# Kernel optimization log

Measured on AMD Instinct MI355X. Metric: run time of the kernel, lower is better.

The kernel has to match this reference:

```python
import jax, jax.numpy as jnp
import numpy as np

B, S, D, H, W = 2, 2048, 1024, 16, 256
HD = D // H

def setup_inputs() -> dict:
    key = jax.random.key(0)
    k1, k2, k3 = jax.random.split(key, 3)
    x = jax.random.normal(k1, (B, S, D), dtype=jnp.float32)
    w_qkv = jax.random.normal(k2, (D, 3 * D), dtype=jnp.float32) * (D ** -0.5)
    b_qkv = jnp.zeros((3 * D,), dtype=jnp.float32)
    w_out = jax.random.normal(k3, (D, D), dtype=jnp.float32) * (D ** -0.5)
    b_out = jnp.zeros((D,), dtype=jnp.float32)
    return {"x": x, "w_qkv": w_qkv, "b_qkv": b_qkv, "w_out": w_out, "b_out": b_out}

def reference(x, w_qkv, b_qkv, w_out, b_out):
    b, s, d = x.shape
    qkv = x @ w_qkv + b_qkv                       # [B,S,3D]
    qkv = qkv.reshape(b, s, 3, H, HD)
    q = jnp.transpose(qkv[:, :, 0], (0, 2, 1, 3))  # [B,H,S,HD]
    k = jnp.transpose(qkv[:, :, 1], (0, 2, 1, 3))
    v = jnp.transpose(qkv[:, :, 2], (0, 2, 1, 3))
    # NOTE: original scales by d_model**0.5, not head_dim**0.5
    scores = jnp.einsum('bhqd,bhkd->bhqk', q, k) / (d ** 0.5)
    idx = jnp.arange(s)
    band = jnp.abs(idx[:, None] - idx[None, :]) <= W  # |i-j| <= window_size
    scores = jnp.where(band[None, None], scores, -jnp.inf)
    attn = jax.nn.softmax(scores, axis=-1)
    out = jnp.einsum('bhqk,bhkd->bhqd', attn, v)
    out = jnp.transpose(out, (0, 2, 1, 3)).reshape(b, s, d)
    return out @ w_out + b_out
```

## Files before the change

kernel.cpp:

```cpp
#include <hip/hip_runtime.h>
#include <cstdint>
#include <cmath>

typedef unsigned short u16;
typedef __attribute__((ext_vector_type(8))) short bf16x8;
typedef __attribute__((ext_vector_type(4))) float f32x4;
typedef __attribute__((ext_vector_type(8))) unsigned short u16x8;
typedef __attribute__((ext_vector_type(4))) unsigned short u16x4;

#define DEV static __device__ __forceinline__

DEV u16 f2bf(float f) {
  union { float f; uint32_t u; } v; v.f = f;
  uint32_t r = (v.u + 0x7fffu + ((v.u >> 16) & 1u)) >> 16;
  return (u16)r;
}

DEV float fexp2(float x) { return exp2f(x); }

DEV void async16(void* lds, const void* g) {
  __builtin_amdgcn_global_load_lds(
      (const __attribute__((address_space(1))) uint32_t*)g,
      (__attribute__((address_space(3))) uint32_t*)lds, 16, 0, 0);
}

#define QSCALE 0.04508422002778011f

__global__ void conv8(const float* __restrict__ in, u16* __restrict__ out, int n8) {
  int i = blockIdx.x * 256 + threadIdx.x;
  if (i >= n8) return;
  const float4* p = (const float4*)in + (size_t)i * 2;
  float4 a = p[0], b = p[1];
  u16x8 ov;
  ov[0] = f2bf(a.x); ov[1] = f2bf(a.y); ov[2] = f2bf(a.z); ov[3] = f2bf(a.w);
  ov[4] = f2bf(b.x); ov[5] = f2bf(b.y); ov[6] = f2bf(b.z); ov[7] = f2bf(b.w);
  *(u16x8*)(out + (size_t)i * 8) = ov;
}

__global__ void tconv(const float* __restrict__ in, u16* __restrict__ out, int R, int Cdim) {
  __shared__ float t[32][33];
  const int tx = threadIdx.x & 31, ty = threadIdx.x >> 5;
  const int r0 = blockIdx.y * 32, c0 = blockIdx.x * 32;
#pragma unroll
  for (int k = 0; k < 4; ++k) {
    int r = ty + k * 8;
    t[r][tx] = in[(size_t)(r0 + r) * Cdim + c0 + tx];
  }
  __syncthreads();
#pragma unroll
  for (int k = 0; k < 4; ++k) {
    int cc = ty + k * 8;
    out[(size_t)(c0 + cc) * R + r0 + tx] = f2bf(t[tx][cc]);
  }
}

template <int EPI>
__global__ __launch_bounds__(256, 2) void gemm_bt(
    const u16* __restrict__ A, const u16* __restrict__ BT,
    const float* __restrict__ bias, float* __restrict__ C,
    u16* __restrict__ qb, u16* __restrict__ kbuf, u16* __restrict__ vtb,
    int Mdim, int Ndim, int Kdim)
{
  __shared__ u16 Alds[128 * 64];
  __shared__ u16 Blds[128 * 64];
  const int tid = threadIdx.x;
  const int wid = tid >> 6, lane = tid & 63;
  const int g = lane >> 4, c = lane & 15;
  const int wr = wid >> 1, wc = wid & 1;
  const int gx = gridDim.x;
  const int nwg = gx * gridDim.y;
  const int lin = blockIdx.y * gx + blockIdx.x;
  const int work = (lin & 7) * (nwg >> 3) + (lin >> 3);
  const int row0 = (work / gx) * 128, col0 = (work % gx) * 128;

  f32x4 acc[4][4] = {};

  for (int kt = 0; kt < Kdim; kt += 64) {
    __syncthreads();
#pragma unroll
    for (int it = 0; it < 4; ++it) {
      int chunk = wid * 256 + it * 64 + lane;
      int r = chunk >> 3, j = chunk & 7;
      int js = j ^ (r & 7);
      async16((char*)Alds + (wid * 256 + it * 64) * 16,
              A + (size_t)(row0 + r) * Kdim + kt + js * 8);
      async16((char*)Blds + (wid * 256 + it * 64) * 16,
              BT + (size_t)(col0 + r) * Kdim + kt + js * 8);
    }
    __syncthreads();
#pragma unroll
    for (int kk = 0; kk < 2; ++kk) {
      bf16x8 av[4], bv[4];
#pragma unroll
      for (int mi = 0; mi < 4; ++mi) {
        int r = wr * 64 + mi * 16 + c;
        int js = (kk * 4 + g) ^ (r & 7);
        av[mi] = *(const bf16x8*)((const char*)Alds + r * 128 + js * 16);
      }
#pragma unroll
      for (int ni = 0; ni < 4; ++ni) {
        int r = wc * 64 + ni * 16 + c;
        int js = (kk * 4 + g) ^ (r & 7);
        bv[ni] = *(const bf16x8*)((const char*)Blds + r * 128 + js * 16);
      }
#pragma unroll
      for (int mi = 0; mi < 4; ++mi)
#pragma unroll
        for (int ni = 0; ni < 4; ++ni)
          acc[mi][ni] = __builtin_amdgcn_mfma_f32_16x16x32_bf16(
              av[mi], bv[ni], acc[mi][ni], 0, 0, 0);
    }
  }

#pragma unroll
  for (int mi = 0; mi < 4; ++mi) {
#pragma unroll
    for (int ni = 0; ni < 4; ++ni) {
      int colg = col0 + wc * 64 + ni * 16 + c;
      float bsv = bias[colg];
      int rowb = row0 + wr * 64 + mi * 16 + g * 4;
      if (EPI == 0) {
#pragma unroll
        for (int r = 0; r < 4; ++r)
          C[(size_t)(rowb + r) * Ndim + colg] = acc[mi][ni][r] + bsv;
      } else {
        int t = colg >> 10, rem = colg & 1023;
        int h = rem >> 6, hd = rem & 63;
        int b = rowb >> 11, s0 = rowb & 2047;
        size_t bho = (size_t)(b * 16 + h);
        if (t == 2) {
          u16x4 pv;
#pragma unroll
          for (int r = 0; r < 4; ++r) pv[r] = f2bf(acc[mi][ni][r] + bsv);
          *(u16x4*)(vtb + (bho * 64 + hd) * 2048 + s0) = pv;
        } else {
          u16* dst = (t == 0) ? qb : kbuf;
          float sc = (t == 0) ? QSCALE : 1.0f;
#pragma unroll
          for (int r = 0; r < 4; ++r)
            dst[(bho * 2048 + (s0 + r)) * 64 + hd] = f2bf((acc[mi][ni][r] + bsv) * sc);
        }
      }
    }
  }
}

__global__ __launch_bounds__(512, 4) void attn_win(
    const u16* __restrict__ qb, const u16* __restrict__ kb,
    const u16* __restrict__ vtb, u16* __restrict__ hb)
{
  constexpr int S = 2048, W = 256;
  __shared__ u16 Klds[3][64 * 64];
  __shared__ u16 Vlds[3][64 * 64];
  __shared__ u16 Plds[8][16 * 64];

  const int tid = threadIdx.x, wid = tid >> 6, lane = tid & 63;
  const int g = lane >> 4, c = lane & 15;
  const int lin = blockIdx.x;
  const int work = (lin & 7) * 64 + (lin >> 3);
  const int qt = work & 15, bh = work >> 4;
  const int q0 = qt * 128;
  const int qr0 = q0 + wid * 16;
  const int qw = qr0 + c;
  const size_t bho = (size_t)bh * S * 64;

  bf16x8 aq[2];
  {
    const u16* qrow = qb + bho + (size_t)qw * 64;
    aq[0] = *(const bf16x8*)(qrow + g * 8);
    aq[1] = *(const bf16x8*)(qrow + 32 + g * 8);
  }
  f32x4 o[4] = {};
  float m = -1e30f, lsum = 0.f;

  const int kstart = (q0 - W > 0) ? (q0 - W) : 0;
  const int kend = (q0 + 128 + W < S) ? (q0 + 128 + W) : S;
  const int ntiles = (kend - kstart) >> 6;

  const int sr = tid >> 3, sj = tid & 7;
  const int sjs = sj ^ (sr & 7);
#define STAGE(buf, k0s)                                                         \
  {                                                                             \
    async16((char*)&Klds[buf][0] + tid * 16,                                    \
            kb + bho + (size_t)((k0s) + sr) * 64 + sjs * 8);                    \
    async16((char*)&Vlds[buf][0] + tid * 16,                                    \
            vtb + bho + (size_t)sr * S + (k0s) + sjs * 8);                      \
  }

  STAGE(0, kstart);
  if (ntiles > 1) STAGE(1, kstart + 64);

  for (int i = 0; i < ntiles; ++i) {
    const int k0 = kstart + (i << 6);
    if (i + 1 < ntiles) { asm volatile("s_waitcnt vmcnt(2)" ::: "memory"); }
    else                { asm volatile("s_waitcnt vmcnt(0)" ::: "memory"); }
    __builtin_amdgcn_s_barrier();
    __builtin_amdgcn_sched_barrier(0);
    if (i + 2 < ntiles) STAGE((i + 2) % 3, k0 + 128);

    const int cur = i % 3;
    const bool wave_active = !(k0 > qr0 + 15 + W) && !(k0 + 63 < qr0 - W);
    if (wave_active) {
      const u16* Kb = &Klds[cur][0];
      const u16* Vb = &Vlds[cur][0];

      f32x4 sacc[4] = {};
      __builtin_amdgcn_s_setprio(1);
#pragma unroll
      for (int kb4 = 0; kb4 < 4; ++kb4) {
        int krow = kb4 * 16 + c;
#pragma unroll
        for (int kk = 0; kk < 2; ++kk) {
          int js = (kk * 4 + g) ^ (krow & 7);
          bf16x8 bk = *(const bf16x8*)((const char*)Kb + krow * 128 + js * 16);
          sacc[kb4] = __builtin_amdgcn_mfma_f32_16x16x32_bf16(bk, aq[kk], sacc[kb4], 0, 0, 0);
        }
      }
      __builtin_amdgcn_s_setprio(0);

      const bool full = (k0 >= qr0 + 15 - W) && (k0 + 63 <= qr0 + W);
      float sl[4][4];
      if (full) {
#pragma unroll
        for (int kb4 = 0; kb4 < 4; ++kb4)
#pragma unroll
          for (int r = 0; r < 4; ++r) sl[kb4][r] = sacc[kb4][r];
      } else {
#pragma unroll
        for (int kb4 = 0; kb4 < 4; ++kb4) {
#pragma unroll
          for (int r = 0; r < 4; ++r) {
            int key = k0 + kb4 * 16 + g * 4 + r;
            int d = qw - key;
            bool valid = (d <= W) && (d >= -W);
            sl[kb4][r] = valid ? sacc[kb4][r] : -1e30f;
          }
        }
      }

      float mx = fmaxf(
          fmaxf(fmaxf(fmaxf(sl[0][0], sl[0][1]), fmaxf(sl[0][2], sl[0][3])),
                fmaxf(fmaxf(sl[1][0], sl[1][1]), fmaxf(sl[1][2], sl[1][3]))),
          fmaxf(fmaxf(fmaxf(sl[2][0], sl[2][1]), fmaxf(sl[2][2], sl[2][3])),
                fmaxf(fmaxf(sl[3][0], sl[3][1]), fmaxf(sl[3][2], sl[3][3]))));
      mx = fmaxf(mx, __shfl_xor(mx, 16));
      mx = fmaxf(mx, __shfl_xor(mx, 32));

      if (!__all(mx - m <= 8.0f)) {
        float mnew = fmaxf(m, mx);
        float fs = fexp2(m - mnew);
        m = mnew;
        lsum *= fs;
        float fsr[4];
#pragma unroll
        for (int r = 0; r < 4; ++r)
          fsr[r] = __shfl(fs, (lane & 48) | (((lane & 48) >> 2) + r));
#pragma unroll
        for (int nb = 0; nb < 4; ++nb)
#pragma unroll
          for (int r = 0; r < 4; ++r) o[nb][r] *= fsr[r];
      }

      float rsum = 0.f;
      u16* Pw = &Plds[wid][0];
#pragma unroll
      for (int kb4 = 0; kb4 < 4; ++kb4) {
        float p0, p1, p2, p3;
        if (full) {
          p0 = fexp2(sl[kb4][0] - m); p1 = fexp2(sl[kb4][1] - m);
          p2 = fexp2(sl[kb4][2] - m); p3 = fexp2(sl[kb4][3] - m);
        } else {
          p0 = (sl[kb4][0] > -1e29f) ? fexp2(sl[kb4][0] - m) : 0.f;
          p1 = (sl[kb4][1] > -1e29f) ? fexp2(sl[kb4][1] - m) : 0.f;
          p2 = (sl[kb4][2] > -1e29f) ? fexp2(sl[kb4][2] - m) : 0.f;
          p3 = (sl[kb4][3] > -1e29f) ? fexp2(sl[kb4][3] - m) : 0.f;
        }
        rsum += (p0 + p1) + (p2 + p3);
        uint32_t lo, hi;
        asm("v_cvt_pk_bf16_f32 %0, %1, %2" : "=v"(lo) : "v"(p0), "v"(p1));
        asm("v_cvt_pk_bf16_f32 %0, %1, %2" : "=v"(hi) : "v"(p2), "v"(p3));
        uint2 wv; wv.x = lo; wv.y = hi;
        *(uint2*)((char*)Pw + c * 128 + (((kb4 * 2 + (g >> 1)) ^ (c & 7)) << 4) +
                  ((g & 1) << 3)) = wv;
      }
      rsum += __shfl_xor(rsum, 16);
      rsum += __shfl_xor(rsum, 32);
      lsum += rsum;

      asm volatile("s_waitcnt lgkmcnt(0)" ::: "memory");
      __builtin_amdgcn_sched_barrier(0);
      __builtin_amdgcn_s_setprio(1);
#pragma unroll
      for (int ks = 0; ks < 2; ++ks) {
        int js = (ks * 4 + g) ^ (c & 7);
        bf16x8 pa = *(const bf16x8*)((const char*)Pw + c * 128 + js * 16);
#pragma unroll
        for (int nb = 0; nb < 4; ++nb) {
          int hd = nb * 16 + c;
          int vjs = (ks * 4 + g) ^ (hd & 7);
          bf16x8 bv = *(const bf16x8*)((const char*)Vb + hd * 128 + vjs * 16);
          o[nb] = __builtin_amdgcn_mfma_f32_16x16x32_bf16(pa, bv, o[nb], 0, 0, 0);
        }
      }
      __builtin_amdgcn_s_setprio(0);
    }
  }
#undef STAGE

  const int b = bh >> 4, h = bh & 15;
  float linv[4];
#pragma unroll
  for (int r = 0; r < 4; ++r)
    linv[r] = 1.0f / __shfl(lsum, (lane & 48) | (((lane & 48) >> 2) + r));
#pragma unroll
  for (int r = 0; r < 4; ++r) {
    int qr = qr0 + g * 4 + r;
#pragma unroll
    for (int nb = 0; nb < 4; ++nb) {
      int col = h * 64 + nb * 16 + c;
      hb[(size_t)(b * 2048 + qr) * 1024 + col] = f2bf(o[nb][r] * linv[r]);
    }
  }
}

extern "C" void kernel_launch(void* const* d_in, const int* in_sizes, int n_in,
                              void* d_out, int out_size, void* d_ws, size_t ws_size,
                              hipStream_t stream) {
  const float* x     = (const float*)d_in[0];
  const float* w_qkv = (const float*)d_in[1];
  const float* b_qkv = (const float*)d_in[2];
  const float* w_out = (const float*)d_in[3];
  const float* b_out = (const float*)d_in[4];
  float* out = (float*)d_out;

  char* ws = (char*)d_ws;
  const size_t MB = 1024 * 1024;
  u16* xbf   = (u16*)(ws);
  u16* wqT   = (u16*)(ws + 8 * MB);
  u16* woT   = (u16*)(ws + 14 * MB);
  u16* qbuf  = (u16*)(ws + 16 * MB);
  u16* kbuf  = (u16*)(ws + 24 * MB);
  u16* vtbuf = (u16*)(ws + 32 * MB);
  u16* hbuf  = (u16*)(ws + 40 * MB);

  conv8<<<dim3(4096 * 1024 / 8 / 256), 256, 0, stream>>>(x, xbf, 4096 * 1024 / 8);
  tconv<<<dim3(3072 / 32, 1024 / 32), 256, 0, stream>>>(w_qkv, wqT, 1024, 3072);
  tconv<<<dim3(1024 / 32, 1024 / 32), 256, 0, stream>>>(w_out, woT, 1024, 1024);
  gemm_bt<1><<<dim3(3072 / 128, 4096 / 128), 256, 0, stream>>>(
      xbf, wqT, b_qkv, nullptr, qbuf, kbuf, vtbuf, 4096, 3072, 1024);
  attn_win<<<dim3(512), 512, 0, stream>>>(qbuf, kbuf, vtbuf, hbuf);
  gemm_bt<0><<<dim3(1024 / 128, 4096 / 128), 256, 0, stream>>>(
      hbuf, woT, b_out, out, nullptr, nullptr, nullptr, 4096, 1024, 1024);
}
```

Measured before the change: 161.9 us.

## Double-buffer GEMM LDS tiles to overlap async global loads with MFMA

The GEMM main loop now uses two LDS buffers per operand and issues the async global-to-LDS loads for the next K tile before computing on the current one, waiting on vmcnt and a barrier only at the end of each iteration. This is meant to hide global load latency behind the MFMA work instead of serialising load and compute. It doubles LDS usage to 64KB per block, which may reduce occupancy under launch_bounds(256,2). The sched_barrier keeps the compiler from reordering the prefetch into the compute.

Measured after the change: 178.9 us. 10.5% more time.

```diff
diff --git a/kernel.cpp b/kernel.cpp
--- a/kernel.cpp
+++ b/kernel.cpp
@@ -61,8 +61,8 @@
     u16* __restrict__ qb, u16* __restrict__ kbuf, u16* __restrict__ vtb,
     int Mdim, int Ndim, int Kdim)
 {
-  __shared__ u16 Alds[128 * 64];
-  __shared__ u16 Blds[128 * 64];
+  __shared__ u16 Alds[2][128 * 64];
+  __shared__ u16 Blds[2][128 * 64];
   const int tid = threadIdx.x;
   const int wid = tid >> 6, lane = tid & 63;
   const int g = lane >> 4, c = lane & 15;
@@ -75,19 +75,27 @@
 
   f32x4 acc[4][4] = {};
 
+#define GSTAGE(buf, kt)                                                     \
+  _Pragma("unroll") for (int it = 0; it < 4; ++it) {                        \
+    int chunk = wid * 256 + it * 64 + lane;                                 \
+    int r = chunk >> 3, j = chunk & 7;                                      \
+    int js = j ^ (r & 7);  \
+    async16((char*)&Alds[buf][0] + chunk * 16,                              \
+            A + (size_t)(row0 + r) * Kdim + (kt) + js * 8);                 \
+    async16((char*)&Blds[buf][0] + chunk * 16,                              \
+            BT + (size_t)(col0 + r) * Kdim + (kt) + js * 8);                \
+  }
+
+  GSTAGE(0, 0);
+  asm volatile("s_waitcnt vmcnt(0)" ::: "memory");
+  __builtin_amdgcn_s_barrier();
+
+  int cur = 0;
   for (int kt = 0; kt < Kdim; kt += 64) {
-    __syncthreads();
-#pragma unroll
-    for (int it = 0; it < 4; ++it) {
-      int chunk = wid * 256 + it * 64 + lane;
-      int r = chunk >> 3, j = chunk & 7;
-      int js = j ^ (r & 7);
-      async16((char*)Alds + (wid * 256 + it * 64) * 16,
-              A + (size_t)(row0 + r) * Kdim + kt + js * 8);
-      async16((char*)Blds + (wid * 256 + it * 64) * 16,
-              BT + (size_t)(col0 + r) * Kdim + kt + js * 8);
-    }
-    __syncthreads();
+    if (kt + 64 < Kdim) GSTAGE(cur ^ 1, kt + 64);
+    __builtin_amdgcn_sched_barrier(0);
+    const u16* Ab = &Alds[cur][0];
+    const u16* Bb = &Blds[cur][0];
 #pragma unroll
     for (int kk = 0; kk < 2; ++kk) {
       bf16x8 av[4], bv[4];
@@ -95,13 +103,13 @@
       for (int mi = 0; mi < 4; ++mi) {
         int r = wr * 64 + mi * 16 + c;
         int js = (kk * 4 + g) ^ (r & 7);
-        av[mi] = *(const bf16x8*)((const char*)Alds + r * 128 + js * 16);
+        av[mi] = *(const bf16x8*)((const char*)Ab + r * 128 + js * 16);
       }
 #pragma unroll
       for (int ni = 0; ni < 4; ++ni) {
         int r = wc * 64 + ni * 16 + c;
         int js = (kk * 4 + g) ^ (r & 7);
-        bv[ni] = *(const bf16x8*)((const char*)Blds + r * 128 + js * 16);
+        bv[ni] = *(const bf16x8*)((const char*)Bb + r * 128 + js * 16);
       }
 #pragma unroll
       for (int mi = 0; mi < 4; ++mi)
@@ -110,7 +118,11 @@
           acc[mi][ni] = __builtin_amdgcn_mfma_f32_16x16x32_bf16(
               av[mi], bv[ni], acc[mi][ni], 0, 0, 0);
     }
-  }
+    asm volatile("s_waitcnt vmcnt(0)" ::: "memory");
+    __builtin_amdgcn_s_barrier();
+    cur ^= 1;
+  }
+#undef GSTAGE
 
 #pragma unroll
   for (int mi = 0; mi < 4; ++mi) {
```
